# Kernel optimization log

Hardware: AMD Instinct MI355X
Metric: run time of the kernel (lower is better)

The kernel has to match this reference:

```python
import jax, jax.numpy as jnp
import numpy as np

N, E, F, FE, L = 12000, 120000, 768, 64, 16
Z = 2 * F + F  # concat(x_i, x_j, e) width = 2304


def setup_inputs() -> dict:
    key = jax.random.key(0)
    ks = jax.random.split(key, 24)
    s = 0.02

    def w(k, shape):
        return jax.random.normal(k, shape, dtype=jnp.float32) * s

    inp = {
        "x": jax.random.normal(ks[0], (N, F), dtype=jnp.float32),
        "e_raw": jax.random.normal(ks[1], (E, FE), dtype=jnp.float32),
        "src": jax.random.randint(ks[2], (E,), 0, N, dtype=jnp.int32),
        "dst": jax.random.randint(ks[3], (E,), 0, N, dtype=jnp.int32),
        "W_pre": w(ks[4], (FE, F)), "b_pre": jnp.zeros((F,), jnp.float32),
        "Wf1": w(ks[5], (Z, F)), "bf1": jnp.zeros((F,), jnp.float32),
        "Ws1": w(ks[6], (Z, F)), "bs1": jnp.zeros((F,), jnp.float32),
        "We1": w(ks[7], (Z, F)), "be1": jnp.zeros((F,), jnp.float32),
        "Wf2": w(ks[8], (Z, F)), "bf2": jnp.zeros((F,), jnp.float32),
        "Ws2": w(ks[9], (Z, F)), "bs2": jnp.zeros((F,), jnp.float32),
        "We2": w(ks[10], (Z, F)), "be2": jnp.zeros((F,), jnp.float32),
        "Wd": w(ks[11], (F, L)), "bd": jnp.zeros((L,), jnp.float32),
    }
    return inp


def _crystal_conv(x, e, src, dst, Wf, bf, Ws, bs, We, be):
    # z_ij = x_i || x_j || e_ij  (targets=dst, sources=src, Spektral convention)
    z = jnp.concatenate([x[dst], x[src], e], axis=-1)  # [E, 2304]
    msg = jax.nn.relu(z @ Ws + bs) * jax.nn.sigmoid(z @ Wf + bf)  # [E, F]
    gate = jax.nn.sigmoid(z @ We + be)  # [E, F] (stored as conv.e)
    agg = jax.ops.segment_sum(msg, dst, num_segments=N)  # scatter-sum to targets
    return x + agg, gate


def reference(x, e_raw, src, dst, W_pre, b_pre, Wf1, bf1, Ws1, bs1, We1, be1,
              Wf2, bf2, Ws2, bs2, We2, be2, Wd, bd):
    e = jnp.tanh(e_raw @ W_pre + b_pre)  # pre_edge Dense(768, tanh)
    # dropout layers are identity at inference
    x1, g1 = _crystal_conv(x, e, src, dst, Wf1, bf1, Ws1, bs1, We1, be1)
    e = e + e * g1
    x2, g2 = _crystal_conv(x1, e, src, dst, Wf2, bf2, Ws2, bs2, We2, be2)
    pooled = jnp.sum(x2, axis=0, keepdims=True)  # GlobalSumPool -> [1, F]
    return jax.nn.softmax(pooled @ Wd + bd, axis=-1)  # [1, n_labels]
```

## Files before the change

kernel.cpp:

```cpp
#include <hip/hip_runtime.h>
#include <stdint.h>

#define EN 120000
#define NN 12000
#define FF 768

typedef __attribute__((ext_vector_type(8))) short short8;
typedef __attribute__((ext_vector_type(4))) float floatx4;
typedef __attribute__((ext_vector_type(2))) float floatx2;
typedef __attribute__((ext_vector_type(2))) long long2v;

#ifdef __has_builtin
#if __has_builtin(__builtin_amdgcn_cvt_pk_f32_fp8) && __has_builtin(__builtin_amdgcn_cvt_f32_fp8)
#define HAS_HW_FP8 1
#endif
#if __has_builtin(__builtin_amdgcn_cvt_pk_fp8_f32)
#define HAS_HW_FP8E 1
#endif
#endif
#ifndef HAS_HW_FP8
#define HAS_HW_FP8 0
#endif
#ifndef HAS_HW_FP8E
#define HAS_HW_FP8E 0
#endif

__device__ __forceinline__ short f2b(float f) {
  union { float f; uint32_t i; } v; v.f = f;
  uint32_t r = (v.i + 0x7fffu + ((v.i >> 16) & 1u)) >> 16;
  return (short)(uint16_t)r;
}
__device__ __forceinline__ float f8tof(uint32_t b) {
  union { uint32_t i; float f; } u;
  u.i = (b & 0x7f) << 20;
  float v = u.f * 0x1p120f;
  return (b & 0x80) ? -v : v;
}
__device__ __forceinline__ uint8_t ftof8(float v) {
#if HAS_HW_FP8E
  return (uint8_t)(__builtin_amdgcn_cvt_pk_fp8_f32(v, v, 0, false) & 0xff);
#else
  union { float f; uint32_t i; } u;
  u.f = fabsf(v) * 0x1p-120f;
  uint32_t r = (u.i + 0x7ffffu + ((u.i >> 20) & 1u)) >> 20;
  if (r > 0x7eu) r = 0x7eu;
  return (uint8_t)(r | ((v < 0.f) ? 0x80u : 0u));
#endif
}
__device__ __forceinline__ floatx2 f8pair(uint32_t u) {
#if HAS_HW_FP8
  return __builtin_amdgcn_cvt_pk_f32_fp8(u, false);
#else
  floatx2 r; r.x = f8tof(u & 0xff); r.y = f8tof((u >> 8) & 0xff); return r;
#endif
}
__device__ __forceinline__ float f8one(uint32_t u) {
#if HAS_HW_FP8
  return __builtin_amdgcn_cvt_f32_fp8(u, 0);
#else
  return f8tof(u & 0xff);
#endif
}
__device__ __forceinline__ float sigm(float x) { return 1.f / (1.f + __expf(-x)); }
__device__ __forceinline__ float tanh_fast(float x) {
  float ax = fabsf(x);
  float t = __expf(-2.f * ax);
  float r = (1.f - t) / (1.f + t);
  return copysignf(r, x);
}
__device__ __forceinline__ void async_ld16(const void* g, void* l) {
  __builtin_amdgcn_global_load_lds(
      (const __attribute__((address_space(1))) void*)g,
      (__attribute__((address_space(3))) void*)l, 16, 0, 0);
}
__device__ __forceinline__ int permk(int n) {
  return (n & ~63) | (((n >> 3) & 3) << 4) | (((n >> 5) & 1) << 3) | (n & 7);
}

template <int NW, int EPI, int F8AB>
__global__ __launch_bounds__(256, 2) void gemm_fused(
    const char* __restrict__ A, int lda,
    const char* __restrict__ Bt, int ldb, int wstride,
    int M, int K,
    void* __restrict__ outP, int ldout,
    const float* __restrict__ bias0, const float* __restrict__ bias1,
    const float* __restrict__ bias2,
    const int* __restrict__ dst, const int* __restrict__ src,
    const uint8_t* __restrict__ Pn, int pstride,
    const uint8_t* __restrict__ eInF8, uint8_t* __restrict__ e2Out,
    float* __restrict__ agg)
{
  __shared__ alignas(16) char lA[64 * 64];
  __shared__ alignas(16) char lB[NW * 128 * 64];

  const int tid  = threadIdx.x;
  const int wave = tid >> 6;
  const int lane = tid & 63;
  const int quad = lane >> 4;
  const int l16  = lane & 15;

  const int gx  = gridDim.x;
  const int nwg = gx * gridDim.y;
  int flat = blockIdx.y * gx + blockIdx.x;
  {
    const int q = nwg >> 3, r = nwg & 7;
    const int xcd = flat & 7, lid = flat >> 3;
    flat = (xcd < r ? xcd * (q + 1) : r * (q + 1) + (xcd - r) * q) + lid;
  }
  const int mBase = (flat / gx) * 64;
  const int nBase = (flat % gx) * 128;

  floatx4 acc[NW][4][2];
#pragma unroll
  for (int w = 0; w < NW; ++w)
#pragma unroll
    for (int mt = 0; mt < 4; ++mt)
#pragma unroll
      for (int nt = 0; nt < 2; ++nt)
#pragma unroll
        for (int r = 0; r < 4; ++r) acc[w][mt][nt][r] = 0.f;

  int i4 = tid >> 2;
  int am = mBase + ((i4 & 12) << 2) + ((i4 >> 4) << 2) + (i4 & 3);
  if (am > M - 1) am = M - 1;
  const char* aSrc = A + (size_t)am * lda + (tid & 3) * 16;

  const char* bSrc[NW * 2];
#pragma unroll
  for (int i = 0; i < NW * 2; ++i) {
    int t2 = tid + i * 256;
    int w  = t2 >> 9;
    int r  = (t2 >> 2) & 127;
    bSrc[i] = Bt + (size_t)w * wstride + (size_t)(nBase + r) * ldb + (t2 & 3) * 16;
  }

  const int Kb = K * (F8AB ? 1 : 2);

  for (int k0 = 0; k0 < Kb; k0 += 64) {
    __syncthreads();
    async_ld16(aSrc + k0, lA + tid * 16);
#pragma unroll
    for (int i = 0; i < NW * 2; ++i)
      async_ld16(bSrc[i] + k0, lB + (tid + i * 256) * 16);
    __syncthreads();

    if constexpr (F8AB) {
      long2v av[4];
#pragma unroll
      for (int mt = 0; mt < 4; ++mt)
        av[mt] = *(const long2v*)(lA + (mt * 16 + l16) * 64 + quad * 16);
#pragma unroll
      for (int w = 0; w < NW; ++w)
#pragma unroll
        for (int nt = 0; nt < 2; ++nt) {
          long2v bv = *(const long2v*)(lB + (w * 128 + wave * 32 + nt * 16 + l16) * 64 + quad * 16);
#pragma unroll
          for (int mt = 0; mt < 4; ++mt) {
            acc[w][mt][nt] = __builtin_amdgcn_mfma_f32_16x16x32_fp8_fp8(
                av[mt].x, bv.x, acc[w][mt][nt], 0, 0, 0);
            acc[w][mt][nt] = __builtin_amdgcn_mfma_f32_16x16x32_fp8_fp8(
                av[mt].y, bv.y, acc[w][mt][nt], 0, 0, 0);
          }
        }
    } else {
      short8 af[4];
#pragma unroll
      for (int mt = 0; mt < 4; ++mt)
        af[mt] = *(const short8*)(lA + (mt * 16 + l16) * 64 + quad * 16);
#pragma unroll
      for (int w = 0; w < NW; ++w)
#pragma unroll
        for (int nt = 0; nt < 2; ++nt) {
          short8 bf = *(const short8*)(lB + (w * 128 + wave * 32 + nt * 16 + l16) * 64 + quad * 16);
#pragma unroll
          for (int mt = 0; mt < 4; ++mt)
            acc[w][mt][nt] = __builtin_amdgcn_mfma_f32_16x16x32_bf16(
                af[mt], bf, acc[w][mt][nt], 0, 0, 0);
        }
    }
  }

  const int colW = nBase + wave * 32;

  float bb0[2], bb1[2], bb2[2];
  if (EPI == 1 || EPI == 2 || EPI == 3) {
#pragma unroll
    for (int nt = 0; nt < 2; ++nt) {
      int n = colW + nt * 16 + l16;
      bb0[nt] = bias0[n];
      if (EPI == 2 || EPI == 3) bb1[nt] = bias1[n];
      if (EPI == 2) bb2[nt] = bias2[n];
    }
  }

  if constexpr (EPI == 2 || EPI == 3) {
    const int n0 = colW + l16;
    const int mQ = mBase + quad * 16;
    int dp = -1;
    float run0 = 0.f, run1 = 0.f;
#pragma unroll
    for (int j = 0; j < 16; ++j) {
      const int mt = j >> 2, r = j & 3;
      const int m = mQ + j;
      const int d = dst[m];
      const int s = src[m];
      const uint8_t* Pd = Pn + (size_t)d * pstride;
      const uint8_t* Ps = Pn + (size_t)s * pstride;
      float msg[2];
#pragma unroll
      for (int nt = 0; nt < 2; ++nt) {
        const int n = n0 + nt * 16;
        uint32_t pt = *(const unsigned short*)(Pd + 2 * n);
        uint32_t pm = *(const unsigned short*)(Ps + 1536 + 2 * n);
        floatx2 vt = f8pair(pt);
        floatx2 vm = f8pair(pm);
        float hf = acc[0][mt][nt][r] + vt.x + vm.x + bb0[nt];
        float hs = acc[1][mt][nt][r] + vt.y + vm.y + bb1[nt];
        msg[nt] = fmaxf(hs, 0.f) * sigm(hf);
        if (EPI == 2) {
          float he = acc[2][mt][nt][r] + f8one(Pd[3072 + n]) + f8one(Ps[3840 + n]) + bb2[nt];
          float ev = f8one(eInF8[(size_t)m * FF + permk(n)]);
          e2Out[(size_t)m * FF + permk(n)] = ftof8(ev * (1.f + sigm(he)));
        }
      }
      if (d != dp) {
        if (dp >= 0) {
          atomicAdd(&agg[(size_t)dp * FF + n0], run0);
          atomicAdd(&agg[(size_t)dp * FF + n0 + 16], run1);
        }
        run0 = 0.f; run1 = 0.f; dp = d;
      }
      run0 += msg[0];
      run1 += msg[1];
    }
    if (dp >= 0) {
      atomicAdd(&agg[(size_t)dp * FF + n0], run0);
      atomicAdd(&agg[(size_t)dp * FF + n0 + 16], run1);
    }
  } else {
#pragma unroll
    for (int mt = 0; mt < 4; ++mt) {
#pragma unroll
      for (int r = 0; r < 4; ++r) {
        int m = mBase + quad * 16 + mt * 4 + r;
        if (m >= M) continue;
#pragma unroll
        for (int nt = 0; nt < 2; ++nt) {
          int n = colW + nt * 16 + l16;
          float v0 = acc[0][mt][nt][r];
          if (EPI == 0) {
            int q = n / 768, j = n - q * 768;
            size_t o;
            if (q < 4) o = (size_t)(((q & 1) ? 1536 : 0) + 2 * j + ((q >> 1) & 1));
            else       o = (size_t)((q == 4) ? (3072 + j) : (3840 + j));
            ((uint8_t*)outP)[(size_t)m * ldout + o] = ftof8(v0);
          } else {
            ((uint8_t*)outP)[(size_t)m * ldout + permk(n)] = ftof8(tanh_fast(v0 + bb0[nt]));
          }
        }
      }
    }
  }
}

__global__ void hist_k(const int* __restrict__ dst, int* __restrict__ cnt) {
  int i = blockIdx.x * 256 + threadIdx.x;
  if (i < EN) atomicAdd(&cnt[dst[i]], 1);
}

__global__ void scan_k(const int* __restrict__ cnt, int* __restrict__ off) {
  __shared__ int part[1024];
  int t = threadIdx.x;
  int base = t * 12;
  int loc[12];
  int s = 0;
#pragma unroll
  for (int j = 0; j < 12; ++j) {
    int idx = base + j;
    int c = idx < NN ? cnt[idx] : 0;
    loc[j] = s; s += c;
  }
  part[t] = s;
  __syncthreads();
  for (int d = 1; d < 1024; d <<= 1) {
    int v = (t >= d) ? part[t - d] : 0;
    __syncthreads();
    part[t] += v;
    __syncthreads();
  }
  int pre = (t == 0) ? 0 : part[t - 1];
#pragma unroll
  for (int j = 0; j < 12; ++j) {
    int idx = base + j;
    if (idx < NN) off[idx] = pre + loc[j];
  }
}

__global__ void scatter_k(const int* __restrict__ dst, int* __restrict__ off,
                          int* __restrict__ perm) {
  int i = blockIdx.x * 256 + threadIdx.x;
  if (i < EN) { int p = atomicAdd(&off[dst[i]], 1); perm[p] = i; }
}

__global__ void permute_k(const int* __restrict__ dst, const int* __restrict__ src,
                          const int* __restrict__ perm, int* __restrict__ dstS,
                          int* __restrict__ srcS) {
  int i = blockIdx.x * 256 + threadIdx.x;
  if (i < EN) { int e = perm[i]; dstS[i] = dst[e]; srcS[i] = src[e]; }
}

__global__ void gather_f2b(const float* __restrict__ e_raw, const int* __restrict__ perm,
                           short* __restrict__ out, int n) {
  int i = blockIdx.x * 256 + threadIdx.x;
  if (i < n) {
    int j = i >> 6, t = i & 63;
    out[i] = f2b(e_raw[(size_t)perm[j] * 64 + t]);
  }
}

__global__ void conv_f2f8(const float* __restrict__ in, uint8_t* __restrict__ out, int n) {
  int i = blockIdx.x * 256 + threadIdx.x;
  if (i < n) {
    int row = i / FF, col = i - row * FF;
    out[(size_t)row * FF + permk(col)] = ftof8(in[i]);
  }
}

__global__ void transpose_wt(const float* __restrict__ in, short* __restrict__ out,
                             int R, int C) {
  __shared__ float t[32][33];
  int c0 = blockIdx.x * 32, r0 = blockIdx.y * 32;
  int tx = threadIdx.x, ty = threadIdx.y;
#pragma unroll
  for (int i = ty; i < 32; i += 8)
    t[i][tx] = in[(size_t)(r0 + i) * C + (c0 + tx)];
  __syncthreads();
#pragma unroll
  for (int i = ty; i < 32; i += 8)
    out[(size_t)(c0 + i) * R + (r0 + tx)] = f2b(t[tx][i]);
}

__global__ void transpose_wt8(const float* __restrict__ in, uint8_t* __restrict__ out,
                              int R, int C) {
  __shared__ float t[32][33];
  int c0 = blockIdx.x * 32, r0 = blockIdx.y * 32;
  int tx = threadIdx.x, ty = threadIdx.y;
#pragma unroll
  for (int i = ty; i < 32; i += 8)
    t[i][tx] = in[(size_t)(r0 + i) * C + (c0 + tx)];
  __syncthreads();
#pragma unroll
  for (int i = ty; i < 32; i += 8)
    out[(size_t)(c0 + i) * R + permk(r0 + tx)] = ftof8(t[tx][i]);
}

__global__ void make_x1(const float* __restrict__ x, float* __restrict__ agg,
                        uint8_t* __restrict__ x1f8, int n) {
  int i = blockIdx.x * 256 + threadIdx.x;
  if (i < n) {
    float v = x[i] + agg[i];
    agg[i] = v;
    int row = i / FF, col = i - row * FF;
    x1f8[(size_t)row * FF + permk(col)] = ftof8(v);
  }
}

__global__ void pool_k(const float* __restrict__ agg, float* __restrict__ pooled) {
  int t = threadIdx.x;
  int r0 = blockIdx.x * 64;
  float s0 = 0.f, s1 = 0.f, s2 = 0.f;
  for (int r = 0; r < 64; ++r) {
    int row = r0 + r;
    if (row >= NN) break;
    size_t base = (size_t)row * FF;
    s0 += agg[base + t];
    s1 += agg[base + t + 256];
    s2 += agg[base + t + 512];
  }
  atomicAdd(&pooled[t], s0);
  atomicAdd(&pooled[t + 256], s1);
  atomicAdd(&pooled[t + 512], s2);
}

__global__ void head_k(const float* __restrict__ pooled, const float* __restrict__ Wd,
                       const float* __restrict__ bd, float* __restrict__ out) {
  int l = threadIdx.x;
  int ll = l & 15;
  float a = 0.f;
  for (int j = 0; j < FF; ++j) a += pooled[j] * Wd[j * 16 + ll];
  a += bd[ll];
  float mx = a;
  for (int off = 8; off; off >>= 1) mx = fmaxf(mx, __shfl_xor(mx, off, 16));
  float ex = __expf(a - mx), sm = ex;
  for (int off = 8; off; off >>= 1) sm += __shfl_xor(sm, off, 16);
  if (l < 16) out[l] = ex / sm;
}

__global__ void sentinel_k(float* __restrict__ out, int n) {
  int i = blockIdx.x * 256 + threadIdx.x;
  if (i < n) out[i] = -1.0f;
}

extern "C" void kernel_launch(void* const* d_in, const int* in_sizes, int n_in,
                              void* d_out, int out_size, void* d_ws, size_t ws_size,
                              hipStream_t stream) {
  const float* x     = (const float*)d_in[0];
  const float* e_raw = (const float*)d_in[1];
  const int*   src   = (const int*)d_in[2];
  const int*   dst   = (const int*)d_in[3];
  const float* W_pre = (const float*)d_in[4];
  const float* b_pre = (const float*)d_in[5];
  const float* Wf1   = (const float*)d_in[6];
  const float* bf1   = (const float*)d_in[7];
  const float* Ws1   = (const float*)d_in[8];
  const float* bs1   = (const float*)d_in[9];
  const float* We1   = (const float*)d_in[10];
  const float* be1   = (const float*)d_in[11];
  const float* Wf2   = (const float*)d_in[12];
  const float* bf2   = (const float*)d_in[13];
  const float* Ws2   = (const float*)d_in[14];
  const float* bs2   = (const float*)d_in[15];
  const float* Wd    = (const float*)d_in[18];
  const float* bd    = (const float*)d_in[19];
  float* out = (float*)d_out;

  char* w = (char*)d_ws;
  size_t off = 0;
  auto take = [&](size_t b) -> void* {
    void* p = w + off;
    off += (b + 255) & ~(size_t)255;
    return p;
  };
  uint8_t* P    = (uint8_t*)take((size_t)NN * 4608);
  float* agg    = (float*)take((size_t)NN * FF * 4);
  uint8_t* xF8  = (uint8_t*)take((size_t)NN * FF);
  uint8_t* e2   = (uint8_t*)take((size_t)EN * FF);
  short* WpreT  = (short*)take((size_t)FF * 64 * 2);
  uint8_t* Wn1T = (uint8_t*)take((size_t)6 * FF * FF);
  uint8_t* Wb1T = (uint8_t*)take((size_t)3 * FF * FF);
  uint8_t* Wn2T = (uint8_t*)take((size_t)4 * FF * FF);
  uint8_t* Wb2T = (uint8_t*)take((size_t)2 * FF * FF);
  float* pooled = (float*)take((size_t)FF * 4);
  int* cnt      = (int*)take((size_t)NN * 4);
  int* boff     = (int*)take((size_t)NN * 4);
  int* perm     = (int*)take((size_t)EN * 4);
  int* dstS     = (int*)take((size_t)EN * 4);
  int* srcS     = (int*)take((size_t)EN * 4);
  const size_t base = off;

  long long avail = (long long)ws_size - (long long)base - 4096;
  long long ecl = avail / 896;
  int Ec = (int)(ecl < 0 ? 0 : ecl);
  Ec &= ~63;
  if (Ec > EN) Ec = EN;
  if (Ec < 64 || n_in < 20) {
    sentinel_k<<<(out_size + 255) / 256, 256, 0, stream>>>(out, out_size);
    return;
  }
  short* erC   = (short*)take((size_t)Ec * 64 * 2);
  uint8_t* eC  = (uint8_t*)take((size_t)Ec * FF);

  hipMemsetAsync(agg, 0, (size_t)NN * FF * 4, stream);
  hipMemsetAsync(pooled, 0, (size_t)FF * 4, stream);
  hipMemsetAsync(cnt, 0, (size_t)NN * 4, stream);

  hist_k<<<(EN + 255) / 256, 256, 0, stream>>>(dst, cnt);
  scan_k<<<1, 1024, 0, stream>>>(cnt, boff);
  scatter_k<<<(EN + 255) / 256, 256, 0, stream>>>(dst, boff, perm);
  permute_k<<<(EN + 255) / 256, 256, 0, stream>>>(dst, src, perm, dstS, srcS);

  conv_f2f8<<<(NN * FF + 255) / 256, 256, 0, stream>>>(x, xF8, NN * FF);

  dim3 tb(32, 8);
  transpose_wt<<<dim3(24, 2), tb, 0, stream>>>(W_pre, WpreT, 64, FF);
  const float* Wc1[3] = {Wf1, Ws1, We1};
  for (int q = 0; q < 3; ++q) {
    for (int h = 0; h < 2; ++h)
      transpose_wt8<<<dim3(24, 24), tb, 0, stream>>>(Wc1[q] + (size_t)h * FF * FF,
                                                     Wn1T + (size_t)(q * 2 + h) * FF * FF, FF, FF);
    transpose_wt8<<<dim3(24, 24), tb, 0, stream>>>(Wc1[q] + (size_t)2 * FF * FF,
                                                   Wb1T + (size_t)q * FF * FF, FF, FF);
  }
  const float* Wc2[2] = {Wf2, Ws2};
  for (int q = 0; q < 2; ++q) {
    for (int h = 0; h < 2; ++h)
      transpose_wt8<<<dim3(24, 24), tb, 0, stream>>>(Wc2[q] + (size_t)h * FF * FF,
                                                     Wn2T + (size_t)(q * 2 + h) * FF * FF, FF, FF);
    transpose_wt8<<<dim3(24, 24), tb, 0, stream>>>(Wc2[q] + (size_t)2 * FF * FF,
                                                   Wb2T + (size_t)q * FF * FF, FF, FF);
  }

  dim3 blk(256);
  const int gy_n = (NN + 63) / 64;

  gemm_fused<1, 0, 1><<<dim3(36, gy_n), blk, 0, stream>>>(
      (const char*)xF8, FF, (const char*)Wn1T, FF, 0, NN, FF, P, 4608,
      nullptr, nullptr, nullptr, nullptr, nullptr, nullptr, 0, nullptr, nullptr, nullptr);

  for (int eo = 0; eo < EN; eo += Ec) {
    int ec = EN - eo < Ec ? EN - eo : Ec;
    gather_f2b<<<(ec * 64 + 255) / 256, 256, 0, stream>>>(e_raw, perm + eo, erC, ec * 64);
    gemm_fused<1, 1, 0><<<dim3(6, ec / 64), blk, 0, stream>>>(
        (const char*)erC, 64 * 2, (const char*)WpreT, 64 * 2, 0, ec, 64, eC, FF,
        b_pre, nullptr, nullptr, nullptr, nullptr, nullptr, 0, nullptr, nullptr, nullptr);
    gemm_fused<3, 2, 1><<<dim3(6, ec / 64), blk, 0, stream>>>(
        (const char*)eC, FF, (const char*)Wb1T, FF, FF * FF, ec, FF, nullptr, 0,
        bf1, bs1, be1, dstS + eo, srcS + eo, P, 4608,
        eC, e2 + (size_t)eo * FF, agg);
  }

  make_x1<<<(NN * FF + 255) / 256, 256, 0, stream>>>(x, agg, xF8, NN * FF);

  gemm_fused<1, 0, 1><<<dim3(24, gy_n), blk, 0, stream>>>(
      (const char*)xF8, FF, (const char*)Wn2T, FF, 0, NN, FF, P, 4608,
      nullptr, nullptr, nullptr, nullptr, nullptr, nullptr, 0, nullptr, nullptr, nullptr);

  gemm_fused<2, 3, 1><<<dim3(6, EN / 64), blk, 0, stream>>>(
      (const char*)e2, FF, (const char*)Wb2T, FF, FF * FF, EN, FF, nullptr, 0,
      bf2, bs2, nullptr, dstS, srcS, P, 4608,
      nullptr, nullptr, agg);

  pool_k<<<(NN + 63) / 64, blk, 0, stream>>>(agg, pooled);

  head_k<<<1, 64, 0, stream>>>(pooled, Wd, bd, out);

  (void)in_sizes; (void)ws_size;
}
```

Baseline: 1.332 ms.

## Repack node projection layout for wider gathers and hoist target loads per segment

The fp8 node-projection buffer is reordered so the two columns each lane needs (n and n+16) for the f/s halves sit in one 32-bit word, and the e-gate pair sits in one 16-bit word. The epilogue then gathers each source row with a single wider load instead of several narrow ones. The target-side (dst) contribution plus bias is loaded only when the destination changes, rather than once per edge. This cuts scattered byte loads in the gather-heavy epilogue, at the cost of a more intricate index mapping in the producer GEMM epilogue.

```diff
diff --git a/kernel.cpp b/kernel.cpp
--- a/kernel.cpp
+++ b/kernel.cpp
@@ -52,6 +52,13 @@
   return __builtin_amdgcn_cvt_pk_f32_fp8(u, false);
 #else
   floatx2 r; r.x = f8tof(u & 0xff); r.y = f8tof((u >> 8) & 0xff); return r;
+#endif
+}
+__device__ __forceinline__ floatx2 f8pair_hi(uint32_t u) {
+#if HAS_HW_FP8
+  return __builtin_amdgcn_cvt_pk_f32_fp8(u, true);
+#else
+  floatx2 r; r.x = f8tof((u >> 16) & 0xff); r.y = f8tof((u >> 24) & 0xff); return r;
 #endif
 }
 __device__ __forceinline__ float f8one(uint32_t u) {
@@ -195,43 +202,55 @@
 
   if constexpr (EPI == 2 || EPI == 3) {
     const int n0 = colW + l16;
+    const int pOff = ((n0 >> 5) << 6) + ((n0 & 15) << 2);
+    const int eOff = ((n0 >> 5) << 5) + ((n0 & 15) << 1);
+    const int pk0 = permk(n0), pk1 = permk(n0 + 16);
     const int mQ = mBase + quad * 16;
     int dp = -1;
     float run0 = 0.f, run1 = 0.f;
+    float fd0 = 0.f, fd1 = 0.f, sd0 = 0.f, sd1 = 0.f, ed0 = 0.f, ed1 = 0.f;
 #pragma unroll
     for (int j = 0; j < 16; ++j) {
       const int mt = j >> 2, r = j & 3;
       const int m = mQ + j;
       const int d = dst[m];
       const int s = src[m];
-      const uint8_t* Pd = Pn + (size_t)d * pstride;
-      const uint8_t* Ps = Pn + (size_t)s * pstride;
-      float msg[2];
-#pragma unroll
-      for (int nt = 0; nt < 2; ++nt) {
-        const int n = n0 + nt * 16;
-        uint32_t pt = *(const unsigned short*)(Pd + 2 * n);
-        uint32_t pm = *(const unsigned short*)(Ps + 1536 + 2 * n);
-        floatx2 vt = f8pair(pt);
-        floatx2 vm = f8pair(pm);
-        float hf = acc[0][mt][nt][r] + vt.x + vm.x + bb0[nt];
-        float hs = acc[1][mt][nt][r] + vt.y + vm.y + bb1[nt];
-        msg[nt] = fmaxf(hs, 0.f) * sigm(hf);
-        if (EPI == 2) {
-          float he = acc[2][mt][nt][r] + f8one(Pd[3072 + n]) + f8one(Ps[3840 + n]) + bb2[nt];
-          float ev = f8one(eInF8[(size_t)m * FF + permk(n)]);
-          e2Out[(size_t)m * FF + permk(n)] = ftof8(ev * (1.f + sigm(he)));
-        }
-      }
       if (d != dp) {
         if (dp >= 0) {
           atomicAdd(&agg[(size_t)dp * FF + n0], run0);
           atomicAdd(&agg[(size_t)dp * FF + n0 + 16], run1);
         }
         run0 = 0.f; run1 = 0.f; dp = d;
+        const uint8_t* Pd = Pn + (size_t)d * pstride;
+        uint32_t td = *(const uint32_t*)(Pd + pOff);
+        floatx2 ta = f8pair(td), tb = f8pair_hi(td);
+        fd0 = ta.x + bb0[0]; sd0 = ta.y + bb1[0];
+        fd1 = tb.x + bb0[1]; sd1 = tb.y + bb1[1];
+        if (EPI == 2) {
+          uint32_t te = *(const unsigned short*)(Pd + 3072 + eOff);
+          floatx2 ea = f8pair(te);
+          ed0 = ea.x + bb2[0]; ed1 = ea.y + bb2[1];
+        }
       }
-      run0 += msg[0];
-      run1 += msg[1];
+      const uint8_t* Ps = Pn + (size_t)s * pstride;
+      uint32_t tm = *(const uint32_t*)(Ps + 1536 + pOff);
+      floatx2 ma = f8pair(tm), mb = f8pair_hi(tm);
+      float hf0 = acc[0][mt][0][r] + ma.x + fd0;
+      float hs0 = acc[1][mt][0][r] + ma.y + sd0;
+      float hf1 = acc[0][mt][1][r] + mb.x + fd1;
+      float hs1 = acc[1][mt][1][r] + mb.y + sd1;
+      run0 += fmaxf(hs0, 0.f) * sigm(hf0);
+      run1 += fmaxf(hs1, 0.f) * sigm(hf1);
+      if (EPI == 2) {
+        uint32_t me = *(const unsigned short*)(Ps + 3840 + eOff);
+        floatx2 ea = f8pair(me);
+        float he0 = acc[2][mt][0][r] + ea.x + ed0;
+        float he1 = acc[2][mt][1][r] + ea.y + ed1;
+        float ev0 = f8one(eInF8[(size_t)m * FF + pk0]);
+        float ev1 = f8one(eInF8[(size_t)m * FF + pk1]);
+        e2Out[(size_t)m * FF + pk0] = ftof8(ev0 * (1.f + sigm(he0)));
+        e2Out[(size_t)m * FF + pk1] = ftof8(ev1 * (1.f + sigm(he1)));
+      }
     }
     if (dp >= 0) {
       atomicAdd(&agg[(size_t)dp * FF + n0], run0);
@@ -250,9 +269,13 @@
           float v0 = acc[0][mt][nt][r];
           if (EPI == 0) {
             int q = n / 768, j = n - q * 768;
+            int h = (j >> 4) & 1;
             size_t o;
-            if (q < 4) o = (size_t)(((q & 1) ? 1536 : 0) + 2 * j + ((q >> 1) & 1));
-            else       o = (size_t)((q == 4) ? (3072 + j) : (3840 + j));
+            if (q < 4)
+              o = (size_t)(((q & 1) ? 1536 : 0) + ((j >> 5) << 6) + ((j & 15) << 2)
+                           + (h << 1) + ((q >> 1) & 1));
+            else
+              o = (size_t)((q == 4 ? 3072 : 3840) + ((j >> 5) << 5) + ((j & 15) << 1) + h);
             ((uint8_t*)outP)[(size_t)m * ldout + o] = ftof8(v0);
           } else {
             ((uint8_t*)outP)[(size_t)m * ldout + permk(n)] = ftof8(tanh_fast(v0 + bb0[nt]));
```

Result: no change. 1.350 ms (+1.4%).
